# Optimization experiments

Hardware: AMD Instinct MI355X
Metric: run time of the kernel (lower is better)

The kernel has to match this reference:

```python
import jax, jax.numpy as jnp
import numpy as np

D = 128      # d_model
H = 8        # n_heads
HD = D // H  # head_dim = 16
E = 256      # n_experts
R = 32       # kv_lora_rank
B, T = 4, 512
EPS = 1e-6


def _dense_init(k, fi, fo):
    s = float(1.0 / np.sqrt(fi))
    return jax.random.uniform(k, (fi, fo), minval=-s, maxval=s, dtype=jnp.float32)


def setup_inputs() -> dict:
    key = jax.random.key(0)
    ks = jax.random.split(key, 16)
    rng = np.random.RandomState(42)
    Q, _ = np.linalg.qr(rng.randn(D, D))
    glim = float(np.sqrt(6.0 / (D + D)))
    return {
        'x': jax.random.normal(ks[0], (B, T, D), dtype=jnp.float32),
        'g1': jnp.ones((D,), jnp.float32),
        'qW': _dense_init(ks[1], D, D), 'qb': jnp.zeros((D,), jnp.float32),
        'kdW': _dense_init(ks[2], D, R), 'kdb': jnp.zeros((R,), jnp.float32),
        'kuW': _dense_init(ks[3], R, 2 * D), 'kub': jnp.zeros((2 * D,), jnp.float32),
        'oW': _dense_init(ks[4], D, D), 'ob': jnp.zeros((D,), jnp.float32),
        'rot': jnp.asarray(Q, jnp.float32),
        'tq_scale': jnp.ones((D,), jnp.float32),
        's1W': _dense_init(ks[5], D, D), 's1b': jnp.zeros((D,), jnp.float32),
        's2W': _dense_init(ks[6], D, D), 's2b': jnp.zeros((D,), jnp.float32),
        'g2': jnp.ones((D,), jnp.float32),
        'gateW': _dense_init(ks[7], D, E), 'gateb': jnp.zeros((E,), jnp.float32),
        'expW': jax.random.uniform(ks[8], (E, D, D), minval=-glim, maxval=glim, dtype=jnp.float32),
        'm1W': _dense_init(ks[9], D, D), 'm1b': jnp.zeros((D,), jnp.float32),
        'm2W': _dense_init(ks[10], D, D), 'm2b': jnp.zeros((D,), jnp.float32),
    }


def _rmsnorm(x, g):
    return g * (x / jnp.sqrt(jnp.mean(x * x, axis=-1, keepdims=True) + EPS))


def _swiglu(x, w1, b1, w2, b2):
    gate = x @ w1 + b1
    return gate * jax.nn.sigmoid(gate) * (x @ w2 + b2)


def _mla(x, qW, qb, kdW, kdb, kuW, kub, oW, ob):
    b, t = x.shape[0], x.shape[1]
    q = (x @ qW + qb).reshape(b, t, H, HD)
    kv = ((x @ kdW + kdb) @ kuW + kub).reshape(b, t, H, 2 * HD)
    k, v = jnp.split(kv, 2, axis=-1)
    q = jax.nn.elu(q) + 1.0
    k = jax.nn.elu(k) + 1.0
    # linear attention: context[b,h,d,e] = sum_t k[b,t,h,d] v[b,t,h,e]
    context = jnp.einsum('bthd,bthe->bhde', k, v)
    out = jnp.einsum('bthd,bhde->bthe', q, context)
    k_sum = jnp.sum(k, axis=1)  # [b,h,d]
    z = 1.0 / (jnp.einsum('bthd,bhd->bth', q, k_sum) + EPS)
    out = out * z[..., None]
    return out.reshape(b, t, D) @ oW + ob


def _turbo_quant(x, rot, scale):
    x = x @ rot
    mag = jnp.sqrt(jnp.mean(x * x, axis=-1, keepdims=True) + EPS)
    phase = x / mag
    qp = jnp.clip(phase * 127.0, -127.0, 127.0) / 127.0
    phase = jax.lax.stop_gradient(qp - phase) + phase  # straight-through
    return phase * mag * scale


def _moe(h, gateW, gateb, expW, m1W, m1b, m2W, m2b):
    gate_scores = jax.nn.softmax(h @ gateW + gateb, axis=-1)  # [B,T,E]
    top_vals, top_idx = jax.lax.top_k(gate_scores, 2)
    top_w = top_vals / (jnp.sum(top_vals, axis=-1, keepdims=True) + EPS)
    # dense all-expert compute as in the original module
    eo = jnp.einsum('btd,edo->bteo', h, expW)  # [B,T,E,D]
    mask = jnp.sum(jax.nn.one_hot(top_idx, E, dtype=h.dtype) * top_w[..., None], axis=2)  # [B,T,E]
    wavg = jnp.einsum('bteo,bte->bto', eo, mask)
    wavg = _swiglu(wavg, m1W, m1b, m2W, m2b)
    diff_sq = jnp.square(eo - wavg[:, :, None, :])
    wvar = jnp.einsum('bteo,bte->bto', diff_sq, mask)
    consensus = jnp.exp(-jnp.mean(wvar, axis=-1))  # [B,T]
    return wavg, consensus


def reference(x, g1, qW, qb, kdW, kdb, kuW, kub, oW, ob, rot, tq_scale,
              s1W, s1b, s2W, s2b, g2, gateW, gateb, expW, m1W, m1b, m2W, m2b):
    attn_out = _turbo_quant(_mla(_rmsnorm(x, g1), qW, qb, kdW, kdb, kuW, kub, oW, ob), rot, tq_scale)
    x = x + _swiglu(attn_out, s1W, s1b, s2W, s2b)
    moe_out, consensus = _moe(_rmsnorm(x, g2), gateW, gateb, expW, m1W, m1b, m2W, m2b)
    return x + moe_out, consensus
```

## Files before the change

kernel.cpp:

```cpp
#include <hip/hip_runtime.h>
#include <hip/hip_bf16.h>
#include <math.h>

static constexpr int Dd   = 128;
static constexpr int NH   = 8;
static constexpr int NE   = 256;
static constexpr int RR   = 32;
static constexpr int TT   = 512;
static constexpr int NTOK = 2048;
static constexpr int TPB  = 4;
static constexpr int SLOTS = 256;
#define EPSF 1e-6f

__device__ __forceinline__ float elu1(float v) { return v > 0.f ? v + 1.f : expf(v); }
__device__ __forceinline__ float sigm(float v) { return 1.f / (1.f + expf(-v)); }

__global__ __launch_bounds__(512) void k_pre(
    const float* __restrict__ x, const float* __restrict__ g1,
    const float* __restrict__ qW, const float* __restrict__ qb,
    const float* __restrict__ kdW, const float* __restrict__ kdb,
    const float* __restrict__ kuW, const float* __restrict__ kub,
    float* __restrict__ qbuf, float* __restrict__ kvbuf,
    float* __restrict__ ctx, float* __restrict__ ksum, int* __restrict__ cnt) {
  const int tid = threadIdx.x;
  const int j = tid & 127, g = tid >> 7;
  const int lane = tid & 63;
  const int n0 = blockIdx.x * TPB;

  __shared__ float4 h1T[128];
  __shared__ float4 part[3][128];
  __shared__ float4 kpart[8][32];
  __shared__ float4 kdT[32];
  __shared__ float4 kupart[256];
  __shared__ float4 rtmp[2];

  if (blockIdx.x == 0) {
    for (int i = tid; i < 32 * 256; i += 512) ctx[i] = 0.f;
    ksum[tid] = 0.f;
    if (tid < 256) cnt[tid] = 0;
  }

  float xv[4];
  if (tid < 128) {
    float v[4];
#pragma unroll
    for (int t = 0; t < 4; t++) { xv[t] = x[(n0 + t) * Dd + j]; v[t] = xv[t] * xv[t]; }
#pragma unroll
    for (int o = 32; o > 0; o >>= 1) {
#pragma unroll
      for (int t = 0; t < 4; t++) v[t] += __shfl_xor(v[t], o, 64);
    }
    if (lane == 0) rtmp[tid >> 6] = make_float4(v[0], v[1], v[2], v[3]);
  }
  __syncthreads();
  if (tid < 128) {
    float g1j = g1[j];
#pragma unroll
    for (int t = 0; t < 4; t++) {
      float ss = ((const float*)&rtmp[0])[t] + ((const float*)&rtmp[1])[t];
      ((float*)&h1T[j])[t] = g1j * xv[t] * rsqrtf(ss * (1.f / 128.f) + EPSF);
    }
  }
  __syncthreads();

  {
    float a0 = 0, a1 = 0, a2 = 0, a3 = 0;
    const float* Wp = qW + (g * 32) * Dd + j;
#pragma unroll 16
    for (int i = 0; i < 32; i++) {
      float4 h4 = h1T[g * 32 + i];
      float w = Wp[i * Dd];
      a0 += h4.x * w; a1 += h4.y * w; a2 += h4.z * w; a3 += h4.w * w;
    }
    if (g) part[g - 1][j] = make_float4(a0, a1, a2, a3);
    __syncthreads();
    if (g == 0) {
      float4 p0 = part[0][j], p1 = part[1][j], p2 = part[2][j];
      float bb = qb[j];
      qbuf[(n0 + 0) * Dd + j] = elu1(a0 + p0.x + p1.x + p2.x + bb);
      qbuf[(n0 + 1) * Dd + j] = elu1(a1 + p0.y + p1.y + p2.y + bb);
      qbuf[(n0 + 2) * Dd + j] = elu1(a2 + p0.z + p1.z + p2.z + bb);
      qbuf[(n0 + 3) * Dd + j] = elu1(a3 + p0.w + p1.w + p2.w + bb);
    }
    __syncthreads();
  }

  if (tid < 256) {
    int col = tid & 31, ksp = tid >> 5;
    float a0 = 0, a1 = 0, a2 = 0, a3 = 0;
    const float* Wp = kdW + (ksp * 16) * RR + col;
#pragma unroll
    for (int i = 0; i < 16; i++) {
      float4 h4 = h1T[ksp * 16 + i];
      float w = Wp[i * RR];
      a0 += h4.x * w; a1 += h4.y * w; a2 += h4.z * w; a3 += h4.w * w;
    }
    kpart[ksp][col] = make_float4(a0, a1, a2, a3);
  }
  __syncthreads();
  if (tid < 32) {
    float bb = kdb[tid];
    float s0 = bb, s1 = bb, s2 = bb, s3 = bb;
#pragma unroll
    for (int k = 0; k < 8; k++) {
      float4 p = kpart[k][tid];
      s0 += p.x; s1 += p.y; s2 += p.z; s3 += p.w;
    }
    kdT[tid] = make_float4(s0, s1, s2, s3);
  }
  __syncthreads();

  {
    int col = tid & 255, kh = tid >> 8;
    float a0 = 0, a1 = 0, a2 = 0, a3 = 0;
    const float* Wp = kuW + (kh * 16) * 256 + col;
#pragma unroll
    for (int r = 0; r < 16; r++) {
      float4 k4 = kdT[kh * 16 + r];
      float w = Wp[r * 256];
      a0 += k4.x * w; a1 += k4.y * w; a2 += k4.z * w; a3 += k4.w * w;
    }
    if (kh) kupart[col] = make_float4(a0, a1, a2, a3);
    __syncthreads();
    if (!kh) {
      float4 p = kupart[col];
      float bb = kub[col];
      bool isk = (col & 31) < 16;
      float v0 = a0 + p.x + bb, v1 = a1 + p.y + bb, v2 = a2 + p.z + bb, v3 = a3 + p.w + bb;
      kvbuf[(n0 + 0) * 256 + col] = isk ? elu1(v0) : v0;
      kvbuf[(n0 + 1) * 256 + col] = isk ? elu1(v1) : v1;
      kvbuf[(n0 + 2) * 256 + col] = isk ? elu1(v2) : v2;
      kvbuf[(n0 + 3) * 256 + col] = isk ? elu1(v3) : v3;
    }
  }
}

__global__ __launch_bounds__(256) void k_ctx(const float* __restrict__ kv,
                                             float* __restrict__ ctx,
                                             float* __restrict__ ksum,
                                             const float* __restrict__ oW,
                                             const float* __restrict__ ob,
                                             const float* __restrict__ rot,
                                             float* __restrict__ oR,
                                             float* __restrict__ bR) {
  const int blk = blockIdx.x;
  const int tid = threadIdx.x;
  if (blk < 256) {
    const int bh = blk >> 3, c = blk & 7;
    const int b = bh >> 3, h = bh & 7;
    const int d = tid >> 4, e = tid & 15;
    __shared__ float sh[64 * 32];
#pragma unroll
    for (int r = 0; r < 8; r++) {
      int lin = r * 256 + tid;
      int tok = lin >> 5, off = lin & 31;
      sh[lin] = kv[((b * TT + c * 64 + tok) * 256) + h * 32 + off];
    }
    __syncthreads();
    float acc = 0.f, ks = 0.f;
#pragma unroll 4
    for (int t = 0; t < 64; t++) {
      float kk = sh[t * 32 + d];
      acc += kk * sh[t * 32 + 16 + e];
      ks += kk;
    }
    atomicAdd(&ctx[bh * 256 + d * 16 + e], acc);
    if (e == 0) atomicAdd(&ksum[bh * 16 + d], ks);
  } else if (blk < 320) {
    int idx = (blk - 256) * 256 + tid;
    int row = idx >> 7, col = idx & 127;
    const float* ow = oW + row * 128;
    float acc = 0.f;
#pragma unroll 8
    for (int k = 0; k < 128; k++) acc += ow[k] * rot[k * 128 + col];
    oR[row * 128 + col] = acc;
  } else {
    if (tid < 128) {
      float acc = 0.f;
#pragma unroll 8
      for (int k = 0; k < 128; k++) acc += ob[k] * rot[k * 128 + tid];
      bR[tid] = acc;
    }
  }
}

__global__ __launch_bounds__(512) void k_mid(
    const float* __restrict__ x, const float* __restrict__ qbuf,
    const float* __restrict__ ctx, const float* __restrict__ ksum,
    const float* __restrict__ oR, const float* __restrict__ bR,
    const float* __restrict__ tqs,
    const float* __restrict__ s1W, const float* __restrict__ s1b,
    const float* __restrict__ s2W, const float* __restrict__ s2b,
    const float* __restrict__ g2, const float* __restrict__ gateW,
    const float* __restrict__ gateb,
    float* __restrict__ xnbuf, float* __restrict__ h2buf,
    float* __restrict__ gw, int* __restrict__ tokslot,
    int* __restrict__ slottok, int* __restrict__ cnt) {
  const int tid = threadIdx.x;
  const int j = tid & 127, g = tid >> 7;
  const int lane = tid & 63;
  const int n0 = blockIdx.x * TPB;
  const int b = n0 >> 9;

  __shared__ float4 bufA[128], bufB[128];
  __shared__ float4 part[3][128];
  __shared__ float4 gpart[256];
  __shared__ float4 rtmp[2];
  __shared__ float wvS[4][4]; __shared__ int wiS[4][4];
  __shared__ float zS[4][4];

  float xres[4];
  if (tid < 128) {
#pragma unroll
    for (int t = 0; t < 4; t++) xres[t] = x[(n0 + t) * Dd + j];
  }

  ((float*)&bufA[j])[g] = qbuf[(n0 + g) * Dd + j];
  __syncthreads();

  if (tid < 128) {
    int h = j >> 4, e = j & 15;
    const float* cpt = ctx + (b * NH + h) * 256;
    const float* kpt = ksum + (b * NH + h) * 16;
    float num[4] = {0, 0, 0, 0}, den[4] = {0, 0, 0, 0};
#pragma unroll
    for (int d = 0; d < 16; d++) {
      float cx = cpt[d * 16 + e], ks = kpt[d];
      float4 q4 = bufA[h * 16 + d];
      num[0] += q4.x * cx; num[1] += q4.y * cx; num[2] += q4.z * cx; num[3] += q4.w * cx;
      den[0] += q4.x * ks; den[1] += q4.y * ks; den[2] += q4.z * ks; den[3] += q4.w * ks;
    }
#pragma unroll
    for (int t = 0; t < 4; t++) ((float*)&bufB[j])[t] = num[t] / (den[t] + EPSF);
  }
  __syncthreads();

  {
    float a0 = 0, a1 = 0, a2 = 0, a3 = 0;
    const float* Wp = oR + (g * 32) * Dd + j;
#pragma unroll 16
    for (int i = 0; i < 32; i++) {
      float4 h4 = bufB[g * 32 + i];
      float w = Wp[i * Dd];
      a0 += h4.x * w; a1 += h4.y * w; a2 += h4.z * w; a3 += h4.w * w;
    }
    if (g) part[g - 1][j] = make_float4(a0, a1, a2, a3);
    __syncthreads();
    float tot[4];
    if (g == 0) {
      float4 p0 = part[0][j], p1 = part[1][j], p2 = part[2][j];
      float bb = bR[j];
      tot[0] = a0 + p0.x + p1.x + p2.x + bb; tot[1] = a1 + p0.y + p1.y + p2.y + bb;
      tot[2] = a2 + p0.z + p1.z + p2.z + bb; tot[3] = a3 + p0.w + p1.w + p2.w + bb;
      float v[4];
#pragma unroll
      for (int t = 0; t < 4; t++) v[t] = tot[t] * tot[t];
#pragma unroll
      for (int o = 32; o > 0; o >>= 1) {
#pragma unroll
        for (int t = 0; t < 4; t++) v[t] += __shfl_xor(v[t], o, 64);
      }
      if (lane == 0) rtmp[tid >> 6] = make_float4(v[0], v[1], v[2], v[3]);
    }
    __syncthreads();
    if (g == 0) {
      float scj = tqs[j];
#pragma unroll
      for (int t = 0; t < 4; t++) {
        float ss = ((const float*)&rtmp[0])[t] + ((const float*)&rtmp[1])[t];
        float mag = sqrtf(ss * (1.f / 128.f) + EPSF);
        float zc = fminf(fmaxf(tot[t], -mag), mag);
        ((float*)&bufA[j])[t] = zc * scj;
      }
    }
    __syncthreads();
  }

  {
    float a0 = 0, a1 = 0, a2 = 0, a3 = 0;
    const float* Wp = (g < 2 ? s1W : s2W) + ((g & 1) * 64) * Dd + j;
#pragma unroll 16
    for (int i = 0; i < 64; i++) {
      float4 h4 = bufA[(g & 1) * 64 + i];
      float w = Wp[i * Dd];
      a0 += h4.x * w; a1 += h4.y * w; a2 += h4.z * w; a3 += h4.w * w;
    }
    if (g) part[g - 1][j] = make_float4(a0, a1, a2, a3);
    __syncthreads();
    if (g == 0) {
      float b1 = s1b[j], b2 = s2b[j];
      float4 p0 = part[0][j], p1 = part[1][j], p2 = part[2][j];
      float gv[4], uv[4], xn[4], v[4];
      gv[0] = a0 + p0.x + b1; gv[1] = a1 + p0.y + b1;
      gv[2] = a2 + p0.z + b1; gv[3] = a3 + p0.w + b1;
      uv[0] = p1.x + p2.x + b2; uv[1] = p1.y + p2.y + b2;
      uv[2] = p1.z + p2.z + b2; uv[3] = p1.w + p2.w + b2;
      float g2j = g2[j];
#pragma unroll
      for (int t = 0; t < 4; t++) {
        xn[t] = xres[t] + gv[t] * sigm(gv[t]) * uv[t];
        xnbuf[(n0 + t) * Dd + j] = xn[t];
        ((float*)&bufB[j])[t] = g2j * xn[t];
        v[t] = xn[t] * xn[t];
      }
#pragma unroll
      for (int o = 32; o > 0; o >>= 1) {
#pragma unroll
        for (int t = 0; t < 4; t++) v[t] += __shfl_xor(v[t], o, 64);
      }
      if (lane == 0) rtmp[tid >> 6] = make_float4(v[0], v[1], v[2], v[3]);
    }
    __syncthreads();
  }

  float val[4];
  float r2[4];
  {
    int col = tid & 255, kh = tid >> 8;
    float a0 = 0, a1 = 0, a2 = 0, a3 = 0;
    const float* Wp = gateW + (kh * 64) * NE + col;
#pragma unroll 16
    for (int i = 0; i < 64; i++) {
      float4 h4 = bufB[kh * 64 + i];
      float w = Wp[i * NE];
      a0 += h4.x * w; a1 += h4.y * w; a2 += h4.z * w; a3 += h4.w * w;
    }
    if (kh) gpart[col] = make_float4(a0, a1, a2, a3);
    __syncthreads();
#pragma unroll
    for (int t = 0; t < 4; t++) {
      float ss = ((const float*)&rtmp[0])[t] + ((const float*)&rtmp[1])[t];
      r2[t] = rsqrtf(ss * (1.f / 128.f) + EPSF);
    }
    if (!kh) {
      float4 p = gpart[col];
      float bb = gateb[col];
      val[0] = (a0 + p.x) * r2[0] + bb; val[1] = (a1 + p.y) * r2[1] + bb;
      val[2] = (a2 + p.z) * r2[2] + bb; val[3] = (a3 + p.w) * r2[3] + bb;
    }
    if (tid < 128) {
#pragma unroll
      for (int t = 0; t < 4; t++)
        h2buf[(n0 + t) * Dd + j] = ((const float*)&bufB[j])[t] * r2[t];
    }
  }
  __syncthreads();

  float m1[4]; int i1[4];
  {
    if (tid < 256) {
      float bv[4]; int bi[4];
#pragma unroll
      for (int t = 0; t < 4; t++) { bv[t] = val[t]; bi[t] = tid; }
#pragma unroll
      for (int o = 32; o > 0; o >>= 1) {
#pragma unroll
        for (int t = 0; t < 4; t++) {
          float wv = __shfl_xor(bv[t], o, 64);
          int wi = __shfl_xor(bi[t], o, 64);
          if (wv > bv[t] || (wv == bv[t] && wi < bi[t])) { bv[t] = wv; bi[t] = wi; }
        }
      }
      if (lane == 0) {
#pragma unroll
        for (int t = 0; t < 4; t++) { wvS[tid >> 6][t] = bv[t]; wiS[tid >> 6][t] = bi[t]; }
      }
    }
    __syncthreads();
    if (tid < 256) {
#pragma unroll
      for (int t = 0; t < 4; t++) {
        m1[t] = wvS[0][t]; i1[t] = wiS[0][t];
#pragma unroll
        for (int w = 1; w < 4; w++) {
          float cv = wvS[w][t]; int ci = wiS[w][t];
          if (cv > m1[t] || (cv == m1[t] && ci < i1[t])) { m1[t] = cv; i1[t] = ci; }
        }
      }
    }
    __syncthreads();
  }
  float m2[4]; int i2[4];
  {
    if (tid < 256) {
      float bv[4]; int bi[4];
#pragma unroll
      for (int t = 0; t < 4; t++) {
        bv[t] = (tid == i1[t]) ? -INFINITY : val[t];
        bi[t] = tid;
      }
#pragma unroll
      for (int o = 32; o > 0; o >>= 1) {
#pragma unroll
        for (int t = 0; t < 4; t++) {
          float wv = __shfl_xor(bv[t], o, 64);
          int wi = __shfl_xor(bi[t], o, 64);
          if (wv > bv[t] || (wv == bv[t] && wi < bi[t])) { bv[t] = wv; bi[t] = wi; }
        }
      }
      if (lane == 0) {
#pragma unroll
        for (int t = 0; t < 4; t++) { wvS[tid >> 6][t] = bv[t]; wiS[tid >> 6][t] = bi[t]; }
      }
    }
    __syncthreads();
    if (tid < 256) {
#pragma unroll
      for (int t = 0; t < 4; t++) {
        m2[t] = wvS[0][t]; i2[t] = wiS[0][t];
#pragma unroll
        for (int w = 1; w < 4; w++) {
          float cv = wvS[w][t]; int ci = wiS[w][t];
          if (cv > m2[t] || (cv == m2[t] && ci < i2[t])) { m2[t] = cv; i2[t] = ci; }
        }
      }
    }
    __syncthreads();
  }
  {
    if (tid < 256) {
      float v[4];
#pragma unroll
      for (int t = 0; t < 4; t++) v[t] = expf(val[t] - m1[t]);
#pragma unroll
      for (int o = 32; o > 0; o >>= 1) {
#pragma unroll
        for (int t = 0; t < 4; t++) v[t] += __shfl_xor(v[t], o, 64);
      }
      if (lane == 0) {
#pragma unroll
        for (int t = 0; t < 4; t++) zS[tid >> 6][t] = v[t];
      }
    }
    __syncthreads();
  }
  if (tid < 4) {
    int t = tid, tok = n0 + t;
    float Z = zS[0][t] + zS[1][t] + zS[2][t] + zS[3][t];
    float p1 = 1.f / Z;
    float p2 = expf(m2[t] - m1[t]) / Z;
    float s = p1 + p2 + EPSF;
    int e1 = i1[t], e2 = i2[t];
    int s1 = atomicAdd(&cnt[e1], 1); if (s1 > SLOTS - 1) s1 = SLOTS - 1;
    int s2 = atomicAdd(&cnt[e2], 1); if (s2 > SLOTS - 1) s2 = SLOTS - 1;
    int sl1 = e1 * SLOTS + s1, sl2 = e2 * SLOTS + s2;
    slottok[sl1] = tok; slottok[sl2] = tok;
    tokslot[tok * 2] = sl1; tokslot[tok * 2 + 1] = sl2;
    gw[tok * 2] = p1 / s; gw[tok * 2 + 1] = p2 / s;
  }
}

__global__ __launch_bounds__(512) void k_exp(const float* __restrict__ h2buf,
                                             const int* __restrict__ slottok,
                                             const int* __restrict__ cnt,
                                             const float* __restrict__ expW,
                                             float* __restrict__ ybuf) {
  const int e = blockIdx.x;
  int n = cnt[e]; if (n > SLOTS) n = SLOTS;
  if (n == 0) return;
  const int base = e * SLOTS;
  const int tid = threadIdx.x;
  const int j = tid & 127, g = tid >> 7;
  __shared__ __align__(16) float hT[128 * 20];
  const float* Wp = expW + (size_t)e * Dd * Dd + j;
  for (int t0 = 0; t0 < n; t0 += 16) {
    int m = n - t0; if (m > 16) m = 16;
    __syncthreads();
    for (int tt = g; tt < m; tt += 4) {
      int tok = slottok[base + t0 + tt];
      hT[j * 20 + tt] = h2buf[tok * Dd + j];
    }
    __syncthreads();
    float acc[4] = {0, 0, 0, 0};
#pragma unroll 8
    for (int i = 0; i < 128; i++) {
      float w = Wp[i * Dd];
      float4 h4 = *(const float4*)&hT[i * 20 + g * 4];
      acc[0] += h4.x * w; acc[1] += h4.y * w; acc[2] += h4.z * w; acc[3] += h4.w * w;
    }
#pragma unroll
    for (int k = 0; k < 4; k++) {
      int tt = g * 4 + k;
      if (tt < m) ybuf[(size_t)(base + t0 + tt) * Dd + j] = acc[k];
    }
  }
}

__global__ __launch_bounds__(512) void k_post(
    const float* __restrict__ xnbuf, const float* __restrict__ ybuf,
    const int* __restrict__ tokslot, const float* __restrict__ gw,
    const float* __restrict__ m1W, const float* __restrict__ m1b,
    const float* __restrict__ m2W, const float* __restrict__ m2b,
    float* __restrict__ out) {
  const int tid = threadIdx.x;
  const int j = tid & 127, g = tid >> 7;
  const int lane = tid & 63;
  const int n0 = blockIdx.x * TPB;

  __shared__ float4 y1T[128], y2T[128], inT[128], sT[128];
  __shared__ float4 part[3][128];
  __shared__ float4 rtmp[2];
  __shared__ int sSlot[4][2];
  __shared__ float sWt[4][2];

  if (tid < 4) {
    sSlot[tid][0] = tokslot[(n0 + tid) * 2];
    sSlot[tid][1] = tokslot[(n0 + tid) * 2 + 1];
    sWt[tid][0] = gw[(n0 + tid) * 2];
    sWt[tid][1] = gw[(n0 + tid) * 2 + 1];
  }
  __syncthreads();

  {
    float y1 = ybuf[(size_t)sSlot[g][0] * Dd + j];
    float y2 = ybuf[(size_t)sSlot[g][1] * Dd + j];
    ((float*)&y1T[j])[g] = y1;
    ((float*)&y2T[j])[g] = y2;
    ((float*)&inT[j])[g] = sWt[g][0] * y1 + sWt[g][1] * y2;
  }
  __syncthreads();

  {
    float a0 = 0, a1 = 0, a2 = 0, a3 = 0;
    const float* Wp = (g < 2 ? m1W : m2W) + ((g & 1) * 64) * Dd + j;
#pragma unroll 16
    for (int i = 0; i < 64; i++) {
      float4 h4 = inT[(g & 1) * 64 + i];
      float w = Wp[i * Dd];
      a0 += h4.x * w; a1 += h4.y * w; a2 += h4.z * w; a3 += h4.w * w;
    }
    if (g) part[g - 1][j] = make_float4(a0, a1, a2, a3);
    __syncthreads();
    if (g == 0) {
      float b1 = m1b[j], b2 = m2b[j];
      float4 p0 = part[0][j], p1 = part[1][j], p2 = part[2][j];
      float gv[4], uv[4];
      gv[0] = a0 + p0.x + b1; gv[1] = a1 + p0.y + b1;
      gv[2] = a2 + p0.z + b1; gv[3] = a3 + p0.w + b1;
      uv[0] = p1.x + p2.x + b2; uv[1] = p1.y + p2.y + b2;
      uv[2] = p1.z + p2.z + b2; uv[3] = p1.w + p2.w + b2;
#pragma unroll
      for (int t = 0; t < 4; t++) {
        float sv = gv[t] * sigm(gv[t]) * uv[t];
        ((float*)&sT[j])[t] = sv;
        out[(n0 + t) * Dd + j] = xnbuf[(n0 + t) * Dd + j] + sv;
      }
    }
    __syncthreads();
  }

  if (tid < 128) {
    float v[4];
#pragma unroll
    for (int t = 0; t < 4; t++) {
      float sv = ((const float*)&sT[j])[t];
      float d1 = ((const float*)&y1T[j])[t] - sv;
      float d2 = ((const float*)&y2T[j])[t] - sv;
      v[t] = sWt[t][0] * d1 * d1 + sWt[t][1] * d2 * d2;
    }
#pragma unroll
    for (int o = 32; o > 0; o >>= 1) {
#pragma unroll
      for (int t = 0; t < 4; t++) v[t] += __shfl_xor(v[t], o, 64);
    }
    if (lane == 0) rtmp[tid >> 6] = make_float4(v[0], v[1], v[2], v[3]);
  }
  __syncthreads();
  if (tid < 4) {
    float s = ((const float*)&rtmp[0])[tid] + ((const float*)&rtmp[1])[tid];
    out[NTOK * Dd + n0 + tid] = expf(-s * (1.f / 128.f));
  }
}

extern "C" void kernel_launch(void* const* d_in, const int* in_sizes, int n_in,
                              void* d_out, int out_size, void* d_ws, size_t ws_size,
                              hipStream_t stream) {
  const float* x   = (const float*)d_in[0];
  const float* g1  = (const float*)d_in[1];
  const float* qW  = (const float*)d_in[2];
  const float* qb  = (const float*)d_in[3];
  const float* kdW = (const float*)d_in[4];
  const float* kdb = (const float*)d_in[5];
  const float* kuW = (const float*)d_in[6];
  const float* kub = (const float*)d_in[7];
  const float* oW  = (const float*)d_in[8];
  const float* ob  = (const float*)d_in[9];
  const float* rot = (const float*)d_in[10];
  const float* tqs = (const float*)d_in[11];
  const float* s1W = (const float*)d_in[12];
  const float* s1b = (const float*)d_in[13];
  const float* s2W = (const float*)d_in[14];
  const float* s2b = (const float*)d_in[15];
  const float* g2  = (const float*)d_in[16];
  const float* gW  = (const float*)d_in[17];
  const float* gb  = (const float*)d_in[18];
  const float* eW  = (const float*)d_in[19];
  const float* m1W = (const float*)d_in[20];
  const float* m1b = (const float*)d_in[21];
  const float* m2W = (const float*)d_in[22];
  const float* m2b = (const float*)d_in[23];
  float* out = (float*)d_out;
  float* ws  = (float*)d_ws;

  float* qbuf   = ws;
  float* kvbuf  = ws + 262144;
  float* ctx    = ws + 786432;
  float* ksum   = ws + 794624;
  float* h2buf  = ws + 795136;
  float* xnbuf  = ws + 1057280;
  float* gw     = ws + 1319424;
  float* oRb    = ws + 1323520;
  float* bRb    = ws + 1339904;
  int*   cnt     = (int*)(ws + 1373056);
  int*   tokslot = (int*)(ws + 1373312);
  int*   slottok = (int*)(ws + 1377408);
  float* ybuf   = ws + 1442944;

  k_pre<<<NTOK / TPB, 512, 0, stream>>>(x, g1, qW, qb, kdW, kdb, kuW, kub,
                                        qbuf, kvbuf, ctx, ksum, cnt);
  k_ctx<<<321, 256, 0, stream>>>(kvbuf, ctx, ksum, oW, ob, rot, oRb, bRb);
  k_mid<<<NTOK / TPB, 512, 0, stream>>>(x, qbuf, ctx, ksum, oRb, bRb, tqs,
                                        s1W, s1b, s2W, s2b, g2, gW, gb,
                                        xnbuf, h2buf, gw, tokslot, slottok, cnt);
  k_exp<<<NE, 512, 0, stream>>>(h2buf, slottok, cnt, eW, ybuf);
  k_post<<<NTOK / TPB, 512, 0, stream>>>(xnbuf, ybuf, tokslot, gw,
                                         m1W, m1b, m2W, m2b, out);
}
```

Before: 165.4 us.

## Fuse all stages into one cooperative persistent kernel with grid syncs

Replaces the five-kernel pipeline with a single cooperative kernel that runs every stage and separates them with grid-wide syncs. The q/k/v activations, the context partials and the routing metadata now stay in shared memory or registers across stages instead of going through global memory. The goal is to remove per-launch overhead and several global round trips. The costs are four grid barriers, a very large shared-memory footprint per block that may cap occupancy, and the requirement that the whole grid be co-resident; the old multi-kernel path is kept as a fallback if the cooperative launch fails.

```diff
diff --git a/kernel.cpp b/kernel.cpp
--- a/kernel.cpp
+++ b/kernel.cpp
@@ -1,19 +1,548 @@
 #include <hip/hip_runtime.h>
-#include <hip/hip_bf16.h>
+#include <hip/hip_cooperative_groups.h>
 #include <math.h>
 
-static constexpr int Dd   = 128;
-static constexpr int NH   = 8;
-static constexpr int NE   = 256;
-static constexpr int RR   = 32;
-static constexpr int TT   = 512;
-static constexpr int NTOK = 2048;
-static constexpr int TPB  = 4;
+namespace cg = cooperative_groups;
+
+static constexpr int Dd    = 128;
+static constexpr int NH    = 8;
+static constexpr int NE    = 256;
+static constexpr int RR    = 32;
+static constexpr int TT    = 512;
+static constexpr int NTOK  = 2048;
 static constexpr int SLOTS = 256;
 #define EPSF 1e-6f
 
 __device__ __forceinline__ float elu1(float v) { return v > 0.f ? v + 1.f : expf(v); }
 __device__ __forceinline__ float sigm(float v) { return 1.f / (1.f + expf(-v)); }
+
+struct Params {
+  const float *x, *g1, *qW, *qb, *kdW, *kdb, *kuW, *kub, *oW, *ob, *rot, *tqs;
+  const float *s1W, *s1b, *s2W, *s2b, *g2, *gateW, *gateb, *expW, *m1W, *m1b, *m2W, *m2b;
+  float *out;
+  float *ctx, *ksum, *h2buf, *oR, *bR, *ybuf;
+  int *cnt, *slottok;
+};
+
+template <int TPB>
+__device__ __forceinline__ void fused_body(const Params P) {
+  constexpr int NG    = TPB / 4;
+  constexpr int GRIDB = NTOK / TPB;
+  constexpr int BPE   = GRIDB / NE;
+  const int tid = threadIdx.x;
+  const int bid = blockIdx.x;
+  const int j = tid & 127, g = tid >> 7;
+  const int lane = tid & 63;
+  const int base_n0 = bid * TPB;
+  const int b = base_n0 >> 9;
+
+  __shared__ float4 h1T[128];
+  __shared__ float4 bufQ[NG][128];
+  __shared__ float4 bufB[128];
+  __shared__ float4 part[3][128];
+  __shared__ float4 kpart[8][32];
+  __shared__ float4 kdT[32];
+  __shared__ float4 kupart[256];
+  __shared__ float4 rtmp[2];
+  __shared__ __align__(16) float kS[NG][8][16][4];
+  __shared__ __align__(16) float vS[NG][8][16][4];
+  __shared__ float wvS[4][4]; __shared__ int wiS[4][4];
+  __shared__ float zS[4][4];
+  __shared__ int sSlot[TPB][2]; __shared__ float sWt[TPB][2];
+  __shared__ __align__(16) float hT[128 * 20];
+  __shared__ float4 y1T[128], y2T[128], inT[128], sT[128];
+
+  float xv[NG][4];
+  float xn[NG][4];
+#pragma unroll
+  for (int grp = 0; grp < NG; grp++)
+#pragma unroll
+    for (int t = 0; t < 4; t++) { xv[grp][t] = 0.f; xn[grp][t] = 0.f; }
+
+  if (bid == 0) {
+    for (int i = tid; i < NH * 4 * 256; i += 512) P.ctx[i] = 0.f;
+    P.ksum[tid] = 0.f;
+    if (tid < NE) P.cnt[tid] = 0;
+  }
+
+  for (int grp = 0; grp < NG; grp++) {
+    const int n0 = base_n0 + grp * 4;
+
+    if (tid < 128) {
+      float v[4];
+#pragma unroll
+      for (int t = 0; t < 4; t++) { xv[grp][t] = P.x[(n0 + t) * Dd + j]; v[t] = xv[grp][t] * xv[grp][t]; }
+#pragma unroll
+      for (int o = 32; o > 0; o >>= 1) {
+#pragma unroll
+        for (int t = 0; t < 4; t++) v[t] += __shfl_xor(v[t], o, 64);
+      }
+      if (lane == 0) rtmp[tid >> 6] = make_float4(v[0], v[1], v[2], v[3]);
+    }
+    __syncthreads();
+    if (tid < 128) {
+      float g1j = P.g1[j];
+#pragma unroll
+      for (int t = 0; t < 4; t++) {
+        float ss = ((const float*)&rtmp[0])[t] + ((const float*)&rtmp[1])[t];
+        ((float*)&h1T[j])[t] = g1j * xv[grp][t] * rsqrtf(ss * (1.f / 128.f) + EPSF);
+      }
+    }
+    __syncthreads();
+
+    {
+      float a0 = 0, a1 = 0, a2 = 0, a3 = 0;
+      const float* Wp = P.qW + (g * 32) * Dd + j;
+#pragma unroll 16
+      for (int i = 0; i < 32; i++) {
+        float4 h4 = h1T[g * 32 + i];
+        float w = Wp[i * Dd];
+        a0 += h4.x * w; a1 += h4.y * w; a2 += h4.z * w; a3 += h4.w * w;
+      }
+      if (g) part[g - 1][j] = make_float4(a0, a1, a2, a3);
+      __syncthreads();
+      if (g == 0) {
+        float4 p0 = part[0][j], p1 = part[1][j], p2 = part[2][j];
+        float bb = P.qb[j];
+        ((float*)&bufQ[grp][j])[0] = elu1(a0 + p0.x + p1.x + p2.x + bb);
+        ((float*)&bufQ[grp][j])[1] = elu1(a1 + p0.y + p1.y + p2.y + bb);
+        ((float*)&bufQ[grp][j])[2] = elu1(a2 + p0.z + p1.z + p2.z + bb);
+        ((float*)&bufQ[grp][j])[3] = elu1(a3 + p0.w + p1.w + p2.w + bb);
+      }
+      __syncthreads();
+    }
+
+    if (tid < 256) {
+      int col = tid & 31, ksp = tid >> 5;
+      float a0 = 0, a1 = 0, a2 = 0, a3 = 0;
+      const float* Wp = P.kdW + (ksp * 16) * RR + col;
+#pragma unroll
+      for (int i = 0; i < 16; i++) {
+        float4 h4 = h1T[ksp * 16 + i];
+        float w = Wp[i * RR];
+        a0 += h4.x * w; a1 += h4.y * w; a2 += h4.z * w; a3 += h4.w * w;
+      }
+      kpart[ksp][col] = make_float4(a0, a1, a2, a3);
+    }
+    __syncthreads();
+    if (tid < 32) {
+      float bb = P.kdb[tid];
+      float s0 = bb, s1 = bb, s2 = bb, s3 = bb;
+#pragma unroll
+      for (int k = 0; k < 8; k++) {
+        float4 p = kpart[k][tid];
+        s0 += p.x; s1 += p.y; s2 += p.z; s3 += p.w;
+      }
+      kdT[tid] = make_float4(s0, s1, s2, s3);
+    }
+    __syncthreads();
+
+    {
+      int col = tid & 255, kh = tid >> 8;
+      float a0 = 0, a1 = 0, a2 = 0, a3 = 0;
+      const float* Wp = P.kuW + (kh * 16) * 256 + col;
+#pragma unroll
+      for (int r = 0; r < 16; r++) {
+        float4 k4 = kdT[kh * 16 + r];
+        float w = Wp[r * 256];
+        a0 += k4.x * w; a1 += k4.y * w; a2 += k4.z * w; a3 += k4.w * w;
+      }
+      if (kh) kupart[col] = make_float4(a0, a1, a2, a3);
+      __syncthreads();
+      if (!kh) {
+        float4 p = kupart[col];
+        float bb = P.kub[col];
+        float v0 = a0 + p.x + bb, v1 = a1 + p.y + bb, v2 = a2 + p.z + bb, v3 = a3 + p.w + bb;
+        int h = col >> 5, off = col & 31;
+        if (off < 16) {
+          kS[grp][h][off][0] = elu1(v0); kS[grp][h][off][1] = elu1(v1);
+          kS[grp][h][off][2] = elu1(v2); kS[grp][h][off][3] = elu1(v3);
+        } else {
+          vS[grp][h][off - 16][0] = v0; vS[grp][h][off - 16][1] = v1;
+          vS[grp][h][off - 16][2] = v2; vS[grp][h][off - 16][3] = v3;
+        }
+      }
+    }
+    __syncthreads();
+  }
+
+  if (bid < 32) {
+    int idx = bid * 512 + tid;
+    int row = idx >> 7, col = idx & 127;
+    const float* ow = P.oW + row * 128;
+    float acc = 0.f;
+#pragma unroll 8
+    for (int k = 0; k < 128; k++) acc += ow[k] * P.rot[k * 128 + col];
+    P.oR[idx] = acc;
+  } else if (bid == 32 && tid < 128) {
+    float acc = 0.f;
+#pragma unroll 8
+    for (int k = 0; k < 128; k++) acc += P.ob[k] * P.rot[k * 128 + tid];
+    P.bR[tid] = acc;
+  }
+
+  cg::this_grid().sync();
+
+  {
+    const int h = tid >> 6;
+    const int d = (tid >> 2) & 15;
+    const int e0 = (tid & 3) * 4;
+    const int bh = b * NH + h;
+    float acc[4] = {0.f, 0.f, 0.f, 0.f};
+    float ks = 0.f;
+#pragma unroll
+    for (int grp = 0; grp < NG; grp++) {
+      float4 k4 = *(const float4*)&kS[grp][h][d][0];
+      ks += k4.x + k4.y + k4.z + k4.w;
+#pragma unroll
+      for (int ee = 0; ee < 4; ee++) {
+        float4 v4 = *(const float4*)&vS[grp][h][e0 + ee][0];
+        acc[ee] += k4.x * v4.x + k4.y * v4.y + k4.z * v4.z + k4.w * v4.w;
+      }
+    }
+    float* cp = P.ctx + bh * 256 + d * 16 + e0;
+#pragma unroll
+    for (int ee = 0; ee < 4; ee++) atomicAdd(cp + ee, acc[ee]);
+    if ((tid & 3) == 0) atomicAdd(&P.ksum[bh * 16 + d], ks);
+  }
+
+  cg::this_grid().sync();
+
+  for (int grp = 0; grp < NG; grp++) {
+    const int n0 = base_n0 + grp * 4;
+    float m1[4]; int i1[4]; float m2[4]; int i2[4];
+    float val[4]; float r2v[4];
+
+    if (tid < 128) {
+      int h = j >> 4, e = j & 15;
+      const float* cpt = P.ctx + (b * NH + h) * 256;
+      const float* kpt = P.ksum + (b * NH + h) * 16;
+      float num[4] = {0, 0, 0, 0}, den[4] = {0, 0, 0, 0};
+#pragma unroll
+      for (int d = 0; d < 16; d++) {
+        float cx = cpt[d * 16 + e], ks = kpt[d];
+        float4 q4 = bufQ[grp][h * 16 + d];
+        num[0] += q4.x * cx; num[1] += q4.y * cx; num[2] += q4.z * cx; num[3] += q4.w * cx;
+        den[0] += q4.x * ks; den[1] += q4.y * ks; den[2] += q4.z * ks; den[3] += q4.w * ks;
+      }
+#pragma unroll
+      for (int t = 0; t < 4; t++) ((float*)&bufB[j])[t] = num[t] / (den[t] + EPSF);
+    }
+    __syncthreads();
+
+    {
+      float a0 = 0, a1 = 0, a2 = 0, a3 = 0;
+      const float* Wp = P.oR + (g * 32) * Dd + j;
+#pragma unroll 16
+      for (int i = 0; i < 32; i++) {
+        float4 h4 = bufB[g * 32 + i];
+        float w = Wp[i * Dd];
+        a0 += h4.x * w; a1 += h4.y * w; a2 += h4.z * w; a3 += h4.w * w;
+      }
+      if (g) part[g - 1][j] = make_float4(a0, a1, a2, a3);
+      __syncthreads();
+      float tot[4];
+      if (g == 0) {
+        float4 p0 = part[0][j], p1 = part[1][j], p2 = part[2][j];
+        float bb = P.bR[j];
+        tot[0] = a0 + p0.x + p1.x + p2.x + bb; tot[1] = a1 + p0.y + p1.y + p2.y + bb;
+        tot[2] = a2 + p0.z + p1.z + p2.z + bb; tot[3] = a3 + p0.w + p1.w + p2.w + bb;
+        float v[4];
+#pragma unroll
+        for (int t = 0; t < 4; t++) v[t] = tot[t] * tot[t];
+#pragma unroll
+        for (int o = 32; o > 0; o >>= 1) {
+#pragma unroll
+          for (int t = 0; t < 4; t++) v[t] += __shfl_xor(v[t], o, 64);
+        }
+        if (lane == 0) rtmp[tid >> 6] = make_float4(v[0], v[1], v[2], v[3]);
+      }
+      __syncthreads();
+      if (g == 0) {
+        float scj = P.tqs[j];
+#pragma unroll
+        for (int t = 0; t < 4; t++) {
+          float ss = ((const float*)&rtmp[0])[t] + ((const float*)&rtmp[1])[t];
+          float mag = sqrtf(ss * (1.f / 128.f) + EPSF);
+          float zc = fminf(fmaxf(tot[t], -mag), mag);
+          ((float*)&bufQ[grp][j])[t] = zc * scj;
+        }
+      }
+      __syncthreads();
+    }
+
+    {
+      float a0 = 0, a1 = 0, a2 = 0, a3 = 0;
+      const float* Wp = (g < 2 ? P.s1W : P.s2W) + ((g & 1) * 64) * Dd + j;
+#pragma unroll 16
+      for (int i = 0; i < 64; i++) {
+        float4 h4 = bufQ[grp][(g & 1) * 64 + i];
+        float w = Wp[i * Dd];
+        a0 += h4.x * w; a1 += h4.y * w; a2 += h4.z * w; a3 += h4.w * w;
+      }
+      if (g) part[g - 1][j] = make_float4(a0, a1, a2, a3);
+      __syncthreads();
+      if (g == 0) {
+        float b1 = P.s1b[j], b2 = P.s2b[j];
+        float4 p0 = part[0][j], p1 = part[1][j], p2 = part[2][j];
+        float gv[4], uv[4], v[4];
+        gv[0] = a0 + p0.x + b1; gv[1] = a1 + p0.y + b1;
+        gv[2] = a2 + p0.z + b1; gv[3] = a3 + p0.w + b1;
+        uv[0] = p1.x + p2.x + b2; uv[1] = p1.y + p2.y + b2;
+        uv[2] = p1.z + p2.z + b2; uv[3] = p1.w + p2.w + b2;
+        float g2j = P.g2[j];
+#pragma unroll
+        for (int t = 0; t < 4; t++) {
+          xn[grp][t] = xv[grp][t] + gv[t] * sigm(gv[t]) * uv[t];
+          ((float*)&bufB[j])[t] = g2j * xn[grp][t];
+          v[t] = xn[grp][t] * xn[grp][t];
+        }
+#pragma unroll
+        for (int o = 32; o > 0; o >>= 1) {
+#pragma unroll
+          for (int t = 0; t < 4; t++) v[t] += __shfl_xor(v[t], o, 64);
+        }
+        if (lane == 0) rtmp[tid >> 6] = make_float4(v[0], v[1], v[2], v[3]);
+      }
+      __syncthreads();
+    }
+
+    {
+      int col = tid & 255, kh = tid >> 8;
+      float a0 = 0, a1 = 0, a2 = 0, a3 = 0;
+      const float* Wp = P.gateW + (kh * 64) * NE + col;
+#pragma unroll 16
+      for (int i = 0; i < 64; i++) {
+        float4 h4 = bufB[kh * 64 + i];
+        float w = Wp[i * NE];
+        a0 += h4.x * w; a1 += h4.y * w; a2 += h4.z * w; a3 += h4.w * w;
+      }
+      if (kh) kupart[col] = make_float4(a0, a1, a2, a3);
+      __syncthreads();
+#pragma unroll
+      for (int t = 0; t < 4; t++) {
+        float ss = ((const float*)&rtmp[0])[t] + ((const float*)&rtmp[1])[t];
+        r2v[t] = rsqrtf(ss * (1.f / 128.f) + EPSF);
+      }
+      if (!kh) {
+        float4 p = kupart[col];
+        float bb = P.gateb[col];
+        val[0] = (a0 + p.x) * r2v[0] + bb; val[1] = (a1 + p.y) * r2v[1] + bb;
+        val[2] = (a2 + p.z) * r2v[2] + bb; val[3] = (a3 + p.w) * r2v[3] + bb;
+      }
+      if (tid < 128) {
+#pragma unroll
+        for (int t = 0; t < 4; t++)
+          P.h2buf[(n0 + t) * Dd + j] = ((const float*)&bufB[j])[t] * r2v[t];
+      }
+    }
+    __syncthreads();
+
+    {
+      if (tid < 256) {
+        float bv[4]; int bi[4];
+#pragma unroll
+        for (int t = 0; t < 4; t++) { bv[t] = val[t]; bi[t] = tid; }
+#pragma unroll
+        for (int o = 32; o > 0; o >>= 1) {
+#pragma unroll
+          for (int t = 0; t < 4; t++) {
+            float wv = __shfl_xor(bv[t], o, 64);
+            int wi = __shfl_xor(bi[t], o, 64);
+            if (wv > bv[t] || (wv == bv[t] && wi < bi[t])) { bv[t] = wv; bi[t] = wi; }
+          }
+        }
+        if (lane == 0) {
+#pragma unroll
+          for (int t = 0; t < 4; t++) { wvS[tid >> 6][t] = bv[t]; wiS[tid >> 6][t] = bi[t]; }
+        }
+      }
+      __syncthreads();
+      if (tid < 256) {
+#pragma unroll
+        for (int t = 0; t < 4; t++) {
+          m1[t] = wvS[0][t]; i1[t] = wiS[0][t];
+#pragma unroll
+          for (int w = 1; w < 4; w++) {
+            float cv = wvS[w][t]; int ci = wiS[w][t];
+            if (cv > m1[t] || (cv == m1[t] && ci < i1[t])) { m1[t] = cv; i1[t] = ci; }
+          }
+        }
+      }
+      __syncthreads();
+    }
+    {
+      if (tid < 256) {
+        float bv[4]; int bi[4];
+#pragma unroll
+        for (int t = 0; t < 4; t++) {
+          bv[t] = (tid == i1[t]) ? -INFINITY : val[t];
+          bi[t] = tid;
+        }
+#pragma unroll
+        for (int o = 32; o > 0; o >>= 1) {
+#pragma unroll
+          for (int t = 0; t < 4; t++) {
+            float wv = __shfl_xor(bv[t], o, 64);
+            int wi = __shfl_xor(bi[t], o, 64);
+            if (wv > bv[t] || (wv == bv[t] && wi < bi[t])) { bv[t] = wv; bi[t] = wi; }
+          }
+        }
+        if (lane == 0) {
+#pragma unroll
+          for (int t = 0; t < 4; t++) { wvS[tid >> 6][t] = bv[t]; wiS[tid >> 6][t] = bi[t]; }
+        }
+      }
+      __syncthreads();
+      if (tid < 256) {
+#pragma unroll
+        for (int t = 0; t < 4; t++) {
+          m2[t] = wvS[0][t]; i2[t] = wiS[0][t];
+#pragma unroll
+          for (int w = 1; w < 4; w++) {
+            float cv = wvS[w][t]; int ci = wiS[w][t];
+            if (cv > m2[t] || (cv == m2[t] && ci < i2[t])) { m2[t] = cv; i2[t] = ci; }
+          }
+        }
+      }
+      __syncthreads();
+    }
+    {
+      if (tid < 256) {
+        float v[4];
+#pragma unroll
+        for (int t = 0; t < 4; t++) v[t] = expf(val[t] - m1[t]);
+#pragma unroll
+        for (int o = 32; o > 0; o >>= 1) {
+#pragma unroll
+          for (int t = 0; t < 4; t++) v[t] += __shfl_xor(v[t], o, 64);
+        }
+        if (lane == 0) {
+#pragma unroll
+          for (int t = 0; t < 4; t++) zS[tid >> 6][t] = v[t];
+        }
+      }
+      __syncthreads();
+    }
+    if (tid < 4) {
+      int t = tid, tok = n0 + t;
+      float Z = zS[0][t] + zS[1][t] + zS[2][t] + zS[3][t];
+      float p1 = 1.f / Z;
+      float p2 = expf(m2[t] - m1[t]) / Z;
+      float s = p1 + p2 + EPSF;
+      int e1 = i1[t], e2 = i2[t];
+      int s1 = atomicAdd(&P.cnt[e1], 1); if (s1 > SLOTS - 1) s1 = SLOTS - 1;
+      int s2 = atomicAdd(&P.cnt[e2], 1); if (s2 > SLOTS - 1) s2 = SLOTS - 1;
+      int sl1 = e1 * SLOTS + s1, sl2 = e2 * SLOTS + s2;
+      P.slottok[sl1] = tok; P.slottok[sl2] = tok;
+      sSlot[grp * 4 + t][0] = sl1; sSlot[grp * 4 + t][1] = sl2;
+      sWt[grp * 4 + t][0] = p1 / s; sWt[grp * 4 + t][1] = p2 / s;
+    }
+    __syncthreads();
+  }
+
+  cg::this_grid().sync();
+
+  {
+    const int e = bid / BPE, sub = bid % BPE;
+    int n = P.cnt[e]; if (n > SLOTS) n = SLOTS;
+    const int base = e * SLOTS;
+    const float* Wp = P.expW + (size_t)e * Dd * Dd + j;
+    for (int t0 = sub * 16; t0 < n; t0 += BPE * 16) {
+      int m = n - t0; if (m > 16) m = 16;
+      __syncthreads();
+      for (int tt = g; tt < m; tt += 4) {
+        int tok = P.slottok[base + t0 + tt];
+        hT[j * 20 + tt] = P.h2buf[tok * Dd + j];
+      }
+      __syncthreads();
+      float acc[4] = {0, 0, 0, 0};
+#pragma unroll 8
+      for (int i = 0; i < 128; i++) {
+        float w = Wp[i * Dd];
+        float4 h4 = *(const float4*)&hT[i * 20 + g * 4];
+        acc[0] += h4.x * w; acc[1] += h4.y * w; acc[2] += h4.z * w; acc[3] += h4.w * w;
+      }
+#pragma unroll
+      for (int k = 0; k < 4; k++) {
+        int tt = g * 4 + k;
+        if (tt < m) P.ybuf[(size_t)(base + t0 + tt) * Dd + j] = acc[k];
+      }
+    }
+  }
+
+  cg::this_grid().sync();
+
+  for (int grp = 0; grp < NG; grp++) {
+    const int n0 = base_n0 + grp * 4;
+    {
+      const int ti = grp * 4 + g;
+      float y1 = P.ybuf[(size_t)sSlot[ti][0] * Dd + j];
+      float y2 = P.ybuf[(size_t)sSlot[ti][1] * Dd + j];
+      ((float*)&y1T[j])[g] = y1;
+      ((float*)&y2T[j])[g] = y2;
+      ((float*)&inT[j])[g] = sWt[ti][0] * y1 + sWt[ti][1] * y2;
+    }
+    __syncthreads();
+
+    {
+      float a0 = 0, a1 = 0, a2 = 0, a3 = 0;
+      const float* Wp = (g < 2 ? P.m1W : P.m2W) + ((g & 1) * 64) * Dd + j;
+#pragma unroll 16
+      for (int i = 0; i < 64; i++) {
+        float4 h4 = inT[(g & 1) * 64 + i];
+        float w = Wp[i * Dd];
+        a0 += h4.x * w; a1 += h4.y * w; a2 += h4.z * w; a3 += h4.w * w;
+      }
+      if (g) part[g - 1][j] = make_float4(a0, a1, a2, a3);
+      __syncthreads();
+      if (g == 0) {
+        float b1 = P.m1b[j], b2 = P.m2b[j];
+        float4 p0 = part[0][j], p1 = part[1][j], p2 = part[2][j];
+        float gv[4], uv[4];
+        gv[0] = a0 + p0.x + b1; gv[1] = a1 + p0.y + b1;
+        gv[2] = a2 + p0.z + b1; gv[3] = a3 + p0.w + b1;
+        uv[0] = p1.x + p2.x + b2; uv[1] = p1.y + p2.y + b2;
+        uv[2] = p1.z + p2.z + b2; uv[3] = p1.w + p2.w + b2;
+#pragma unroll
+        for (int t = 0; t < 4; t++) {
+          float sv = gv[t] * sigm(gv[t]) * uv[t];
+          ((float*)&sT[j])[t] = sv;
+          P.out[(n0 + t) * Dd + j] = xn[grp][t] + sv;
+        }
+      }
+      __syncthreads();
+    }
+
+    if (tid < 128) {
+      float v[4];
+#pragma unroll
+      for (int t = 0; t < 4; t++) {
+        float sv = ((const float*)&sT[j])[t];
+        float d1 = ((const float*)&y1T[j])[t] - sv;
+        float d2 = ((const float*)&y2T[j])[t] - sv;
+        v[t] = sWt[grp * 4 + t][0] * d1 * d1 + sWt[grp * 4 + t][1] * d2 * d2;
+      }
+#pragma unroll
+      for (int o = 32; o > 0; o >>= 1) {
+#pragma unroll
+        for (int t = 0; t < 4; t++) v[t] += __shfl_xor(v[t], o, 64);
+      }
+      if (lane == 0) rtmp[tid >> 6] = make_float4(v[0], v[1], v[2], v[3]);
+    }
+    __syncthreads();
+    if (tid < 4) {
+      float s = ((const float*)&rtmp[0])[tid] + ((const float*)&rtmp[1])[tid];
+      P.out[NTOK * Dd + n0 + tid] = expf(-s * (1.f / 128.f));
+    }
+    __syncthreads();
+  }
+}
+
+__global__ __launch_bounds__(512, 4) void k_fused4(Params P) { fused_body<4>(P); }
+__global__ __launch_bounds__(512)    void k_fused8(Params P) { fused_body<8>(P); }
+
+static constexpr int TPBo = 4;
 
 __global__ __launch_bounds__(512) void k_pre(
     const float* __restrict__ x, const float* __restrict__ g1,
@@ -25,7 +554,7 @@
   const int tid = threadIdx.x;
   const int j = tid & 127, g = tid >> 7;
   const int lane = tid & 63;
-  const int n0 = blockIdx.x * TPB;
+  const int n0 = blockIdx.x * TPBo;
 
   __shared__ float4 h1T[128];
   __shared__ float4 part[3][128];
@@ -199,7 +728,7 @@
   const int tid = threadIdx.x;
   const int j = tid & 127, g = tid >> 7;
   const int lane = tid & 63;
-  const int n0 = blockIdx.x * TPB;
+  const int n0 = blockIdx.x * TPBo;
   const int b = n0 >> 9;
 
   __shared__ float4 bufA[128], bufB[128];
@@ -495,7 +1024,7 @@
   const int tid = threadIdx.x;
   const int j = tid & 127, g = tid >> 7;
   const int lane = tid & 63;
-  const int n0 = blockIdx.x * TPB;
+  const int n0 = blockIdx.x * TPBo;
 
   __shared__ float4 y1T[128], y2T[128], inT[128], sT[128];
   __shared__ float4 part[3][128];
@@ -575,32 +1104,65 @@
 extern "C" void kernel_launch(void* const* d_in, const int* in_sizes, int n_in,
                               void* d_out, int out_size, void* d_ws, size_t ws_size,
                               hipStream_t stream) {
-  const float* x   = (const float*)d_in[0];
-  const float* g1  = (const float*)d_in[1];
-  const float* qW  = (const float*)d_in[2];
-  const float* qb  = (const float*)d_in[3];
-  const float* kdW = (const float*)d_in[4];
-  const float* kdb = (const float*)d_in[5];
-  const float* kuW = (const float*)d_in[6];
-  const float* kub = (const float*)d_in[7];
-  const float* oW  = (const float*)d_in[8];
-  const float* ob  = (const float*)d_in[9];
-  const float* rot = (const float*)d_in[10];
-  const float* tqs = (const float*)d_in[11];
-  const float* s1W = (const float*)d_in[12];
-  const float* s1b = (const float*)d_in[13];
-  const float* s2W = (const float*)d_in[14];
-  const float* s2b = (const float*)d_in[15];
-  const float* g2  = (const float*)d_in[16];
-  const float* gW  = (const float*)d_in[17];
-  const float* gb  = (const float*)d_in[18];
-  const float* eW  = (const float*)d_in[19];
-  const float* m1W = (const float*)d_in[20];
-  const float* m1b = (const float*)d_in[21];
-  const float* m2W = (const float*)d_in[22];
-  const float* m2b = (const float*)d_in[23];
-  float* out = (float*)d_out;
-  float* ws  = (float*)d_ws;
+  float* ws = (float*)d_ws;
+
+  Params p;
+  p.x   = (const float*)d_in[0];
+  p.g1  = (const float*)d_in[1];
+  p.qW  = (const float*)d_in[2];
+  p.qb  = (const float*)d_in[3];
+  p.kdW = (const float*)d_in[4];
+  p.kdb = (const float*)d_in[5];
+  p.kuW = (const float*)d_in[6];
+  p.kub = (const float*)d_in[7];
+  p.oW  = (const float*)d_in[8];
+  p.ob  = (const float*)d_in[9];
+  p.rot = (const float*)d_in[10];
+  p.tqs = (const float*)d_in[11];
+  p.s1W = (const float*)d_in[12];
+  p.s1b = (const float*)d_in[13];
+  p.s2W = (const float*)d_in[14];
+  p.s2b = (const float*)d_in[15];
+  p.g2  = (const float*)d_in[16];
+  p.gateW = (const float*)d_in[17];
+  p.gateb = (const float*)d_in[18];
+  p.expW  = (const float*)d_in[19];
+  p.m1W = (const float*)d_in[20];
+  p.m1b = (const float*)d_in[21];
+  p.m2W = (const float*)d_in[22];
+  p.m2b = (const float*)d_in[23];
+  p.out = (float*)d_out;
+
+  p.ctx     = ws;
+  p.ksum    = ws + 8192;
+  p.oR      = ws + 8704;
+  p.bR      = ws + 25088;
+  p.h2buf   = ws + 25216;
+  p.cnt     = (int*)(ws + 287360);
+  p.slottok = (int*)(ws + 287616);
+  p.ybuf    = ws + 353152;
+
+  void* args[] = {(void*)&p};
+  hipError_t err = hipErrorUnknown;
+
+  int nb4 = 0;
+  if (hipOccupancyMaxActiveBlocksPerMultiprocessor(
+          &nb4, reinterpret_cast<const void*>(&k_fused4), 512, 0) != hipSuccess)
+    nb4 = 0;
+  if (nb4 >= 2) {
+    err = hipLaunchCooperativeKernel((void*)k_fused4, dim3(NTOK / 4), dim3(512),
+                                     args, 0u, stream);
+  }
+  if (err != hipSuccess) {
+    int nb8 = 0;
+    if (hipOccupancyMaxActiveBlocksPerMultiprocessor(
+            &nb8, reinterpret_cast<const void*>(&k_fused8), 512, 0) == hipSuccess &&
+        nb8 >= 1) {
+      err = hipLaunchCooperativeKernel((void*)k_fused8, dim3(NTOK / 8), dim3(512),
+                                       args, 0u, stream);
+    }
+  }
+  if (err == hipSuccess) return;
 
   float* qbuf   = ws;
   float* kvbuf  = ws + 262144;
@@ -616,13 +1178,13 @@
   int*   slottok = (int*)(ws + 1377408);
   float* ybuf   = ws + 1442944;
 
-  k_pre<<<NTOK / TPB, 512, 0, stream>>>(x, g1, qW, qb, kdW, kdb, kuW, kub,
-                                        qbuf, kvbuf, ctx, ksum, cnt);
-  k_ctx<<<321, 256, 0, stream>>>(kvbuf, ctx, ksum, oW, ob, rot, oRb, bRb);
-  k_mid<<<NTOK / TPB, 512, 0, stream>>>(x, qbuf, ctx, ksum, oRb, bRb, tqs,
-                                        s1W, s1b, s2W, s2b, g2, gW, gb,
-                                        xnbuf, h2buf, gw, tokslot, slottok, cnt);
-  k_exp<<<NE, 512, 0, stream>>>(h2buf, slottok, cnt, eW, ybuf);
-  k_post<<<NTOK / TPB, 512, 0, stream>>>(xnbuf, ybuf, tokslot, gw,
-                                         m1W, m1b, m2W, m2b, out);
+  k_pre<<<NTOK / 4, 512, 0, stream>>>(p.x, p.g1, p.qW, p.qb, p.kdW, p.kdb, p.kuW, p.kub,
+                                      qbuf, kvbuf, ctx, ksum, cnt);
+  k_ctx<<<321, 256, 0, stream>>>(kvbuf, ctx, ksum, p.oW, p.ob, p.rot, oRb, bRb);
+  k_mid<<<NTOK / 4, 512, 0, stream>>>(p.x, qbuf, ctx, ksum, oRb, bRb, p.tqs,
+                                      p.s1W, p.s1b, p.s2W, p.s2b, p.g2, p.gateW, p.gateb,
+                                      xnbuf, h2buf, gw, tokslot, slottok, cnt);
+  k_exp<<<NE, 512, 0, stream>>>(h2buf, slottok, cnt, p.expW, ybuf);
+  k_post<<<NTOK / 4, 512, 0, stream>>>(xnbuf, ybuf, tokslot, gw,
+                                       p.m1W, p.m1b, p.m2W, p.m2b, p.out);
 }
```

After: 166.6 us. No clear change (+0.7%).
